# Kernel optimization log

Measured on AMD Instinct MI355X. Metric: run time of the kernel, lower is better.

The kernel has to match this reference:

```python
import jax, jax.numpy as jnp
import numpy as np

# Dimensions (see shape_source)
B, L, D, H = 2, 2048, 768, 12   # batch, seq_len, hidden, heads (bert-base)
E, T, W = 32, 8, 4               # entities per doc, triggers = first T entities, span width
R, N = 57, 20                    # relation types, NOTA embeddings

# Static (trigger, object) pair index lists: s in [0,T), o in [0,E), s != o  -> P = T*(E-1)
_s = np.repeat(np.arange(T), E)
_o = np.tile(np.arange(E), T)
_keep = _s != _o
S_IDX = jnp.asarray(_s[_keep])   # [P]
O_IDX = jnp.asarray(_o[_keep])   # [P]
P = int(_keep.sum())             # 248


def setup_inputs() -> dict:
    key = jax.random.key(0)
    k1, k2, k3, k4, k5 = jax.random.split(key, 5)
    return {
        "sequence_output": jax.random.normal(k1, (B, L, D), jnp.float32),
        # attention weights are nonnegative (post-softmax) -> uniform fill
        "attention": jax.random.uniform(k2, (B, H, L, L), jnp.float32),
        "relation_embeddings": jax.random.normal(k3, (R, 3 * D), jnp.float32),
        "nota_embeddings": jax.random.normal(k4, (N, 3 * D), jnp.float32),
        "span_starts": jax.random.randint(k5, (B, E), 0, L - W, dtype=jnp.int32),
    }


def reference(sequence_output, attention, relation_embeddings, nota_embeddings, span_starts):
    # Span token indices: [B, E, W]
    idx = span_starts[..., None] + jnp.arange(W)
    b_ix = jnp.arange(B)[:, None, None]

    # Ragged span mean-pooling of token embeddings -> entity embeddings [B, E, D]
    ent_emb = sequence_output[b_ix, idx].mean(axis=2)

    # Mean over span tokens of attention rows -> per-entity attention [B, E, H, L]
    att_t = attention.transpose(0, 2, 1, 3)          # [B, L, H, L]
    ent_att = att_t[b_ix, idx].mean(axis=2)          # [B, E, H, L]

    # Localized context per (trigger s, object o) pair:
    # A = A_s * A_o ; q = sum over heads ; a = q / q.sum() ; c = H^T a
    A = ent_att[:, S_IDX] * ent_att[:, O_IDX]        # [B, P, H, L]
    q = A.sum(axis=2)                                 # [B, P, L]
    a = q / q.sum(axis=-1, keepdims=True)             # [B, P, L]
    c = jnp.einsum('bpl,bld->bpd', a, sequence_output)  # [B, P, D]

    # concat(e_s, e_o, c) -> [B, P, 3D]
    embs = jnp.concatenate([ent_emb[:, S_IDX], ent_emb[:, O_IDX], c], axis=-1)

    # Relation scoring against learned codebooks
    scores = embs @ relation_embeddings.T             # [B, P, R]
    nota_scores = (embs @ nota_embeddings.T).max(axis=-1, keepdims=True)  # [B, P, 1]
    return jnp.concatenate([nota_scores, scores], axis=-1)  # [B, P, R+1]
```

## Files before the change

### kernel.cpp

```cpp
#include <hip/hip_runtime.h>
#include <hip/hip_bf16.h>
#include <math.h>

#define BB 2
#define LL 2048
#define DD 768
#define D3 2304
#define HH 12
#define EE 32
#define RR 57
#define NN 20
#define PP 248
#define MM 256
#define KS 8
#define KCH (LL / KS)
#define R80 80
#define NSL 40

#define ENT_EMB_OFF 0
#define A16_OFF   (BB * EE * DD)
#define A16_F     (BB * MM * LL / 2)
#define CPART_OFF (A16_OFF + A16_F)
#define CPART_F   (KS * BB * MM * DD / 2)
#define CODE16_OFF (CPART_OFF + CPART_F)
#define CODE16_F  (R80 * D3 / 2)
#define QSUM_OFF  (CODE16_OFF + CODE16_F)
#define SPART_OFF (QSUM_OFF + 512)

#define NQBLK (BB * 256)
#define NEBLK (EE * BB)
#define NCBLK 8
#define ASTRIDE 388

#define NGBLK 768
#define NQSB 16

typedef __attribute__((ext_vector_type(8))) short bf16x8;
typedef __attribute__((ext_vector_type(4))) float f32x4;

__device__ __forceinline__ unsigned short f2bf(float f) {
    __hip_bfloat16 h = __float2bfloat16(f);
    return __builtin_bit_cast(unsigned short, h);
}
__device__ __forceinline__ float bf2f(unsigned short u) {
    unsigned int x = ((unsigned int)u) << 16;
    return __builtin_bit_cast(float, x);
}
__device__ __forceinline__ void pair_so(int p, int& s, int& o) {
    s = p / 31;
    int r = p - s * 31;
    o = (r < s) ? r : r + 1;
}
__device__ __forceinline__ float dot4(float4 a, float4 b) {
    return a.x * b.x + a.y * b.y + a.z * b.z + a.w * b.w;
}
__device__ __forceinline__ void cast8(float4 u0, float4 u1, short* dst) {
    ushort4 a = make_ushort4(f2bf(u0.x), f2bf(u0.y), f2bf(u0.z), f2bf(u0.w));
    ushort4 b = make_ushort4(f2bf(u1.x), f2bf(u1.y), f2bf(u1.z), f2bf(u1.w));
    *(ushort4*)dst = a;
    *(ushort4*)(dst + 4) = b;
}

__global__ __launch_bounds__(256) void kP(const float* __restrict__ seq,
                                          const float* __restrict__ att,
                                          const float* __restrict__ rel,
                                          const float* __restrict__ nota,
                                          const int* __restrict__ spans,
                                          float* __restrict__ ws) {
    __shared__ __align__(16) float att_s[8][ASTRIDE];
    __shared__ int sp_s[EE];
    int bid = blockIdx.x;
    int t = threadIdx.x;

    if (bid < NQBLK) {
        int xcd = bid & 7, i = bid >> 3;
        int chunk = xcd * (NQBLK / 8) + i;
        int b = chunk >> 8, l0 = (chunk & 255) * 8;
        if (t < EE) sp_s[t] = spans[b * EE + t];
        __syncthreads();
        float4 vv[12];
        #pragma unroll
        for (int it = 0; it < 3; ++it) {
            int i2 = t + it * 256;
            int seg = i2 & 1, eh = i2 >> 1;
            int e = eh / HH, h = eh - e * HH;
            const float* base = att + ((size_t)(b * HH + h) * LL + sp_s[e]) * LL + l0 + seg * 4;
            vv[it * 4 + 0] = *(const float4*)base;
            vv[it * 4 + 1] = *(const float4*)(base + LL);
            vv[it * 4 + 2] = *(const float4*)(base + 2 * LL);
            vv[it * 4 + 3] = *(const float4*)(base + 3 * LL);
        }
        #pragma unroll
        for (int it = 0; it < 3; ++it) {
            int i2 = t + it * 256;
            int seg = i2 & 1, eh = i2 >> 1;
            float4 v0 = vv[it * 4 + 0], v1 = vv[it * 4 + 1];
            float4 v2 = vv[it * 4 + 2], v3 = vv[it * 4 + 3];
            att_s[seg * 4 + 0][eh] = 0.25f * (v0.x + v1.x + v2.x + v3.x);
            att_s[seg * 4 + 1][eh] = 0.25f * (v0.y + v1.y + v2.y + v3.y);
            att_s[seg * 4 + 2][eh] = 0.25f * (v0.z + v1.z + v2.z + v3.z);
            att_s[seg * 4 + 3][eh] = 0.25f * (v0.w + v1.w + v2.w + v3.w);
        }
        __syncthreads();
        int p = t, s, o;
        pair_so(p, s, o);
        float q[8];
        #pragma unroll
        for (int l = 0; l < 8; ++l) {
            float4 a0 = *(const float4*)&att_s[l][s * HH];
            float4 a1 = *(const float4*)&att_s[l][s * HH + 4];
            float4 a2 = *(const float4*)&att_s[l][s * HH + 8];
            float4 b0 = *(const float4*)&att_s[l][o * HH];
            float4 b1 = *(const float4*)&att_s[l][o * HH + 4];
            float4 b2 = *(const float4*)&att_s[l][o * HH + 8];
            q[l] = dot4(a0, b0) + dot4(a1, b1) + dot4(a2, b2);
        }
        unsigned short* A16 = (unsigned short*)(ws + A16_OFF) + (size_t)(b * MM + p) * LL + l0;
        #pragma unroll
        for (int i2 = 0; i2 < 2; ++i2) {
            ushort4 ov = make_ushort4(f2bf(q[i2 * 4 + 0]), f2bf(q[i2 * 4 + 1]),
                                      f2bf(q[i2 * 4 + 2]), f2bf(q[i2 * 4 + 3]));
            *(ushort4*)(A16 + i2 * 4) = ov;
        }
    } else if (bid < NQBLK + NEBLK) {
        int bx = bid - NQBLK;
        int e = bx & 31, b = bx >> 5;
        int st = spans[b * EE + e];
        float* ee = ws + ENT_EMB_OFF + (size_t)(b * EE + e) * DD;
        const float* srow = seq + (size_t)(b * LL + st) * DD;
        for (int d = t; d < DD; d += 256) {
            ee[d] = 0.25f * (srow[d] + srow[DD + d] + srow[2 * DD + d] + srow[3 * DD + d]);
        }
    } else {
        int cid = bid - NQBLK - NEBLK;
        unsigned short* code16 = (unsigned short*)(ws + CODE16_OFF);
        for (int idx = t; idx < 10 * (D3 / 4); idx += 256) {
            int rl = idx / (D3 / 4), dg = idx - rl * (D3 / 4);
            int r = cid * 10 + rl;
            ushort4 ov;
            if (r < RR) {
                float4 v = *(const float4*)(rel + (size_t)r * D3 + dg * 4);
                ov = make_ushort4(f2bf(v.x), f2bf(v.y), f2bf(v.z), f2bf(v.w));
            } else if (r < RR + NN) {
                float4 v = *(const float4*)(nota + (size_t)(r - RR) * D3 + dg * 4);
                ov = make_ushort4(f2bf(v.x), f2bf(v.y), f2bf(v.z), f2bf(v.w));
            } else {
                ov = make_ushort4(0, 0, 0, 0);
            }
            *(ushort4*)(code16 + (size_t)r * D3 + dg * 4) = ov;
        }
    }
}

__global__ __launch_bounds__(256) void k3_gemm(const float* __restrict__ seq,
                                               float* __restrict__ ws) {
    int g = blockIdx.x;
    int t = threadIdx.x;
    int w = t >> 6, lane = t & 63;

    if (g < NGBLK) {
        int m0 = (g & 3) * 64;
        int n0 = ((g >> 2) % 12) * 64;
        int z = g / 48;
        int ks = z & 7, b = z >> 3;
        const unsigned short* A = (const unsigned short*)(ws + A16_OFF) + (size_t)b * MM * LL;
        const float* seqb = seq + (size_t)b * LL * DD;
        int wr = w >> 1, wc = w & 1;
        int fr = lane & 15, kb = lane >> 4;
        int mbase = m0 + wr * 32, nbase = n0 + wc * 32;
        f32x4 acc[2][2] = {};
        int k0c = ks * KCH;
        for (int st = 0; st < 8; ++st) {
            int kk = k0c + st * 32 + kb * 8;
            bf16x8 af[2];
            #pragma unroll
            for (int i = 0; i < 2; ++i)
                af[i] = *(const bf16x8*)(A + (size_t)(mbase + i * 16 + fr) * LL + kk);
            bf16x8 bfv[2];
            #pragma unroll
            for (int j = 0; j < 2; ++j) {
                int n = nbase + j * 16 + fr;
                const float* sp2 = seqb + (size_t)kk * DD + n;
                #pragma unroll
                for (int r = 0; r < 8; ++r)
                    bfv[j][r] = (short)f2bf(sp2[(size_t)r * DD]);
            }
            #pragma unroll
            for (int i = 0; i < 2; ++i)
                #pragma unroll
                for (int j = 0; j < 2; ++j)
                    acc[i][j] = __builtin_amdgcn_mfma_f32_16x16x32_bf16(
                        af[i], bfv[j], acc[i][j], 0, 0, 0);
        }
        unsigned short* cp =
            (unsigned short*)(ws + CPART_OFF) + (size_t)((ks * BB + b) * MM) * DD;
        #pragma unroll
        for (int i = 0; i < 2; ++i)
            #pragma unroll
            for (int j = 0; j < 2; ++j)
                #pragma unroll
                for (int r = 0; r < 4; ++r) {
                    int gm = m0 + wr * 32 + i * 16 + kb * 4 + r;
                    int gn = n0 + wc * 32 + j * 16 + fr;
                    cp[(size_t)gm * DD + gn] = f2bf(acc[i][j][r]);
                }
    } else {
        int qb = g - NGBLK;
        const unsigned short* A16 = (const unsigned short*)(ws + A16_OFF);
        #pragma unroll
        for (int i = 0; i < 8; ++i) {
            int m = qb * 32 + w * 8 + i;
            const unsigned short* rowp = A16 + (size_t)m * LL + lane * 32;
            float v = 0.f;
            #pragma unroll
            for (int u = 0; u < 4; ++u) {
                uint4 x = *(const uint4*)(rowp + u * 8);
                const unsigned short* xs = (const unsigned short*)&x;
                #pragma unroll
                for (int e = 0; e < 8; ++e) v += bf2f(xs[e]);
            }
            #pragma unroll
            for (int off = 32; off > 0; off >>= 1) v += __shfl_xor(v, off, 64);
            if (lane == 0) ws[QSUM_OFF + m] = 1.0f / v;
        }
    }
}

__global__ __launch_bounds__(256) void k4b(float* __restrict__ ws) {
    __shared__ __align__(16) short As[64][200];
    __shared__ __align__(16) short Bs[6][R80][40];
    int mt = blockIdx.x, sl = blockIdx.y;
    int b = mt >> 2, p0 = (mt & 3) * 64;
    int t = threadIdx.x;
    int w = t >> 6, lane = t & 63, fr = lane & 15, kb = lane >> 4;
    int row = t >> 2, sg = t & 3;
    int seg, d0, ls = 0, dgb;
    if (sl < 4)      { seg = 0; d0 = sl * 192;                              dgb = 0; }
    else if (sl < 8) { seg = 1; d0 = (sl - 4) * 192;                        dgb = DD; }
    else             { seg = 2; ls = (sl - 8) >> 2; d0 = ((sl - 8) & 3) * 192; dgb = 2 * DD; }
    int p = p0 + row, s_, o_;
    pair_so(p, s_, o_);
    int asrc = (seg == 0) ? s_ : o_;
    const unsigned short* code16 = (const unsigned short*)(ws + CODE16_OFF);
    const unsigned short* cp16 = (const unsigned short*)(ws + CPART_OFF);
    #pragma unroll
    for (int kk = 0; kk < 6; ++kk) {
        int d = d0 + kk * 32;
        if (seg < 2) {
            const float* src = ws + ENT_EMB_OFF + (size_t)(b * EE + asrc) * DD + d + sg * 8;
            cast8(*(const float4*)src, *(const float4*)(src + 4), &As[row][kk * 32 + sg * 8]);
        } else {
            *(uint4*)&As[row][kk * 32 + sg * 8] =
                *(const uint4*)(cp16 + (size_t)((ls * BB + b) * MM + p) * DD + d + sg * 8);
        }
    }
    for (int i = t; i < 6 * R80 * 4; i += 256) {
        int kk = i / (R80 * 4);
        int rem = i - kk * (R80 * 4);
        int br = rem >> 2, bsg = rem & 3;
        *(uint4*)&Bs[kk][br][bsg * 8] =
            *(const uint4*)(code16 + (size_t)br * D3 + dgb + d0 + kk * 32 + bsg * 8);
    }
    __syncthreads();
    f32x4 acc[5] = {};
    #pragma unroll
    for (int kk = 0; kk < 6; ++kk) {
        bf16x8 af = *(bf16x8*)&As[w * 16 + fr][kk * 32 + kb * 8];
        #pragma unroll
        for (int j = 0; j < 5; ++j) {
            bf16x8 bf = *(bf16x8*)&Bs[kk][j * 16 + fr][kb * 8];
            acc[j] = __builtin_amdgcn_mfma_f32_16x16x32_bf16(af, bf, acc[j], 0, 0, 0);
        }
    }
    float* sp = ws + SPART_OFF;
    #pragma unroll
    for (int j = 0; j < 5; ++j)
        #pragma unroll
        for (int r = 0; r < 4; ++r) {
            int lm = mt * 64 + w * 16 + kb * 4 + r;
            int lr = j * 16 + fr;
            sp[((size_t)lm * NSL + sl) * R80 + lr] = acc[j][r];
        }
}

__global__ __launch_bounds__(256) void kF(const float* __restrict__ ws,
                                          float* __restrict__ out) {
    __shared__ float nota_s[2][NN];
    int pt2 = blockIdx.x, b = blockIdx.y;
    int t = threadIdx.x;
    if (t < 2 * 77) {
        int j = (t < 77) ? 0 : 1;
        int r = (t < 77) ? t : t - 77;
        int p = pt2 * 2 + j;
        int m = b * MM + p;
        const float* sp = ws + SPART_OFF + (size_t)m * NSL * R80 + r;
        float raw = 0.f, csum = 0.f;
        #pragma unroll
        for (int sl = 0; sl < 8; ++sl) raw += sp[(size_t)sl * R80];
        #pragma unroll
        for (int sl = 8; sl < NSL; ++sl) csum += sp[(size_t)sl * R80];
        float v = raw + ws[QSUM_OFF + m] * csum;
        if (r < RR) out[(size_t)(b * PP + p) * (RR + 1) + 1 + r] = v;
        else nota_s[j][r - RR] = v;
    }
    __syncthreads();
    if (t < 2) {
        float mx = -INFINITY;
        #pragma unroll
        for (int n = 0; n < NN; ++n) mx = fmaxf(mx, nota_s[t][n]);
        out[(size_t)(b * PP + pt2 * 2 + t) * (RR + 1)] = mx;
    }
}

extern "C" void kernel_launch(void* const* d_in, const int* in_sizes, int n_in,
                              void* d_out, int out_size, void* d_ws, size_t ws_size,
                              hipStream_t stream) {
    const float* seq   = (const float*)d_in[0];
    const float* att   = (const float*)d_in[1];
    const float* rel   = (const float*)d_in[2];
    const float* nota  = (const float*)d_in[3];
    const int*   spans = (const int*)d_in[4];
    float* ws  = (float*)d_ws;
    float* out = (float*)d_out;

    kP<<<NQBLK + NEBLK + NCBLK, 256, 0, stream>>>(seq, att, rel, nota, spans, ws);
    k3_gemm<<<NGBLK + NQSB, 256, 0, stream>>>(seq, ws);
    k4b<<<dim3(8, NSL), 256, 0, stream>>>(ws);
    kF<<<dim3(PP / 2, BB), 256, 0, stream>>>(ws, out);
}
```

Before: 44.88 us.

## Reduce score slices with atomics in GEMM epilogue instead of partial buffer

The scoring GEMM now scales context-slice partials by the inverse q-sum and atomically adds them straight into the output and a small NOTA accumulator, replacing the large per-slice partial buffer and the reduction pass. The prep kernel gains blocks that zero the output and accumulator, and the final kernel shrinks to a max over NOTA scores. The attention gather loop is also changed from fully unrolled register-staged loads to a simple loop. This trades the partial-buffer write and read traffic for atomic contention across 40 slices, and makes the float summation order nondeterministic.

```diff
diff --git a/kernel.cpp b/kernel.cpp
--- a/kernel.cpp
+++ b/kernel.cpp
@@ -25,15 +25,18 @@
 #define CODE16_OFF (CPART_OFF + CPART_F)
 #define CODE16_F  (R80 * D3 / 2)
 #define QSUM_OFF  (CODE16_OFF + CODE16_F)
-#define SPART_OFF (QSUM_OFF + 512)
+#define SACC_OFF  (QSUM_OFF + 512)
 
 #define NQBLK (BB * 256)
 #define NEBLK (EE * BB)
 #define NCBLK 8
+#define NZBLK 4
 #define ASTRIDE 388
 
 #define NGBLK 768
 #define NQSB 16
+
+#define OUT_F (BB * PP * (RR + 1))
 
 typedef __attribute__((ext_vector_type(8))) short bf16x8;
 typedef __attribute__((ext_vector_type(4))) float f32x4;
@@ -66,7 +69,8 @@
                                           const float* __restrict__ rel,
                                           const float* __restrict__ nota,
                                           const int* __restrict__ spans,
-                                          float* __restrict__ ws) {
+                                          float* __restrict__ ws,
+                                          float* __restrict__ out) {
     __shared__ __align__(16) float att_s[8][ASTRIDE];
     __shared__ int sp_s[EE];
     int bid = blockIdx.x;
@@ -78,24 +82,14 @@
         int b = chunk >> 8, l0 = (chunk & 255) * 8;
         if (t < EE) sp_s[t] = spans[b * EE + t];
         __syncthreads();
-        float4 vv[12];
-        #pragma unroll
-        for (int it = 0; it < 3; ++it) {
-            int i2 = t + it * 256;
+        for (int i2 = t; i2 < EE * HH * 2; i2 += 256) {
             int seg = i2 & 1, eh = i2 >> 1;
             int e = eh / HH, h = eh - e * HH;
             const float* base = att + ((size_t)(b * HH + h) * LL + sp_s[e]) * LL + l0 + seg * 4;
-            vv[it * 4 + 0] = *(const float4*)base;
-            vv[it * 4 + 1] = *(const float4*)(base + LL);
-            vv[it * 4 + 2] = *(const float4*)(base + 2 * LL);
-            vv[it * 4 + 3] = *(const float4*)(base + 3 * LL);
-        }
-        #pragma unroll
-        for (int it = 0; it < 3; ++it) {
-            int i2 = t + it * 256;
-            int seg = i2 & 1, eh = i2 >> 1;
-            float4 v0 = vv[it * 4 + 0], v1 = vv[it * 4 + 1];
-            float4 v2 = vv[it * 4 + 2], v3 = vv[it * 4 + 3];
+            float4 v0 = *(const float4*)base;
+            float4 v1 = *(const float4*)(base + LL);
+            float4 v2 = *(const float4*)(base + 2 * LL);
+            float4 v3 = *(const float4*)(base + 3 * LL);
             att_s[seg * 4 + 0][eh] = 0.25f * (v0.x + v1.x + v2.x + v3.x);
             att_s[seg * 4 + 1][eh] = 0.25f * (v0.y + v1.y + v2.y + v3.y);
             att_s[seg * 4 + 2][eh] = 0.25f * (v0.z + v1.z + v2.z + v3.z);
@@ -131,7 +125,7 @@
         for (int d = t; d < DD; d += 256) {
             ee[d] = 0.25f * (srow[d] + srow[DD + d] + srow[2 * DD + d] + srow[3 * DD + d]);
         }
-    } else {
+    } else if (bid < NQBLK + NEBLK + NCBLK) {
         int cid = bid - NQBLK - NEBLK;
         unsigned short* code16 = (unsigned short*)(ws + CODE16_OFF);
         for (int idx = t; idx < 10 * (D3 / 4); idx += 256) {
@@ -149,6 +143,14 @@
             }
             *(ushort4*)(code16 + (size_t)r * D3 + dg * 4) = ov;
         }
+    } else {
+        int zid = bid - NQBLK - NEBLK - NCBLK;
+        int per_out = (OUT_F + NZBLK - 1) / NZBLK;
+        for (int i = zid * per_out + t; i < min((zid + 1) * per_out, OUT_F); i += 256)
+            out[i] = 0.f;
+        int per_sa = (512 * NN + NZBLK - 1) / NZBLK;
+        for (int i = zid * per_sa + t; i < min((zid + 1) * per_sa, 512 * NN); i += 256)
+            ws[SACC_OFF + i] = 0.f;
     }
 }
 
@@ -226,7 +228,8 @@
     }
 }
 
-__global__ __launch_bounds__(256) void k4b(float* __restrict__ ws) {
+__global__ __launch_bounds__(256) void k4b(float* __restrict__ ws,
+                                           float* __restrict__ out) {
     __shared__ __align__(16) short As[64][200];
     __shared__ __align__(16) short Bs[6][R80][40];
     int mt = blockIdx.x, sl = blockIdx.y;
@@ -272,43 +275,37 @@
             acc[j] = __builtin_amdgcn_mfma_f32_16x16x32_bf16(af, bf, acc[j], 0, 0, 0);
         }
     }
-    float* sp = ws + SPART_OFF;
     #pragma unroll
-    for (int j = 0; j < 5; ++j)
-        #pragma unroll
-        for (int r = 0; r < 4; ++r) {
-            int lm = mt * 64 + w * 16 + kb * 4 + r;
+    for (int r = 0; r < 4; ++r) {
+        int lp = p0 + w * 16 + kb * 4 + r;
+        if (lp >= PP) continue;
+        int lm = b * MM + lp;
+        float qs = (seg == 2) ? ws[QSUM_OFF + lm] : 1.0f;
+        #pragma unroll
+        for (int j = 0; j < 5; ++j) {
             int lr = j * 16 + fr;
-            sp[((size_t)lm * NSL + sl) * R80 + lr] = acc[j][r];
-        }
-}
-
-__global__ __launch_bounds__(256) void kF(const float* __restrict__ ws,
+            float v = acc[j][r] * qs;
+            if (lr < RR) {
+                atomicAdd(&out[(size_t)(b * PP + lp) * (RR + 1) + 1 + lr], v);
+            } else if (lr < RR + NN) {
+                atomicAdd(&ws[SACC_OFF + (size_t)lm * NN + (lr - RR)], v);
+            }
+        }
+    }
+}
+
+__global__ __launch_bounds__(128) void kF(const float* __restrict__ ws,
                                           float* __restrict__ out) {
-    __shared__ float nota_s[2][NN];
-    int pt2 = blockIdx.x, b = blockIdx.y;
+    int half = blockIdx.x, b = blockIdx.y;
     int t = threadIdx.x;
-    if (t < 2 * 77) {
-        int j = (t < 77) ? 0 : 1;
-        int r = (t < 77) ? t : t - 77;
-        int p = pt2 * 2 + j;
+    int p = half * 124 + t;
+    if (t < 124) {
         int m = b * MM + p;
-        const float* sp = ws + SPART_OFF + (size_t)m * NSL * R80 + r;
-        float raw = 0.f, csum = 0.f;
-        #pragma unroll
-        for (int sl = 0; sl < 8; ++sl) raw += sp[(size_t)sl * R80];
-        #pragma unroll
-        for (int sl = 8; sl < NSL; ++sl) csum += sp[(size_t)sl * R80];
-        float v = raw + ws[QSUM_OFF + m] * csum;
-        if (r < RR) out[(size_t)(b * PP + p) * (RR + 1) + 1 + r] = v;
-        else nota_s[j][r - RR] = v;
-    }
-    __syncthreads();
-    if (t < 2) {
+        const float* sa = ws + SACC_OFF + (size_t)m * NN;
         float mx = -INFINITY;
         #pragma unroll
-        for (int n = 0; n < NN; ++n) mx = fmaxf(mx, nota_s[t][n]);
-        out[(size_t)(b * PP + pt2 * 2 + t) * (RR + 1)] = mx;
+        for (int n = 0; n < NN; ++n) mx = fmaxf(mx, sa[n]);
+        out[(size_t)(b * PP + p) * (RR + 1)] = mx;
     }
 }
 
@@ -323,8 +320,8 @@
     float* ws  = (float*)d_ws;
     float* out = (float*)d_out;
 
-    kP<<<NQBLK + NEBLK + NCBLK, 256, 0, stream>>>(seq, att, rel, nota, spans, ws);
+    kP<<<NQBLK + NEBLK + NCBLK + NZBLK, 256, 0, stream>>>(seq, att, rel, nota, spans, ws, out);
     k3_gemm<<<NGBLK + NQSB, 256, 0, stream>>>(seq, ws);
-    k4b<<<dim3(8, NSL), 256, 0, stream>>>(ws);
-    kF<<<dim3(PP / 2, BB), 256, 0, stream>>>(ws, out);
-}
+    k4b<<<dim3(8, NSL), 256, 0, stream>>>(ws, out);
+    kF<<<dim3(2, BB), 128, 0, stream>>>(ws, out);
+}
```

Result: slower. 57.11 us (+27.3%).
